# Performance work log

Measured on AMD Instinct MI355X. Metric: run time of the kernel, lower is better.

## Reference

```python
import math
import jax, jax.numpy as jnp
import numpy as np

FACTOR = 2  # init kwarg of AutoCorrelation


def setup_inputs() -> dict:
    key0 = jax.random.key(0)
    kq, kk, kv = jax.random.split(key0, 3)
    B, H, L, D = 8, 8, 2048, 64
    return {
        "query": jax.random.normal(kq, (B, H, L, D), dtype=jnp.float32),
        "key": jax.random.normal(kk, (B, H, L, D), dtype=jnp.float32),
        "value": jax.random.normal(kv, (B, H, L, D), dtype=jnp.float32),
    }


def reference(query, key, value):
    # Inference (eval-mode) path of AutoCorrelation.forward.
    B, H, L, D = query.shape
    L_KV = key.shape[2]
    # _pad_or_truncate_key_value: match key/value length to query length
    if L > L_KV:
        pad = [(0, 0), (0, 0), (0, L - L_KV), (0, 0)]
        key = jnp.pad(key, pad)
        value = jnp.pad(value, pad)
    else:
        key = key[:, :, :L, :]
        value = value[:, :, :L, :]

    # _period_based_dependency: circular cross-correlation via FFT
    qf = jnp.fft.rfft(jnp.swapaxes(query, -2, -1), axis=-1)   # (B,H,D,L//2+1) complex
    kf = jnp.fft.rfft(jnp.swapaxes(key, -2, -1), axis=-1)
    corr = jnp.fft.irfft(qf * jnp.conj(kf), n=L, axis=-1)     # (B,H,D,L)

    # _time_delay_aggregation (eval branch: per-batch topk delays)
    mean_corr = corr.mean(axis=(1, 2))                         # (B,L)
    num_delays = min(FACTOR * math.ceil(math.log(L)), L)
    w, delay_idx = jax.lax.top_k(mean_corr, num_delays)       # (B,k)
    w = jax.nn.softmax(w, axis=-1)

    ar = jnp.arange(L)

    def body(ctx, inp):
        d, wk = inp  # (B,), (B,)
        idx = (ar[None, :] + d[:, None]) % L                   # (B,L) — circular shift == gather from doubled value
        gathered = jnp.take_along_axis(
            value, jnp.broadcast_to(idx[:, None, :, None], value.shape), axis=2
        )                                                      # (B,H,L,D)
        return ctx + wk[:, None, None, None] * gathered, None

    ctx0 = jnp.zeros_like(value)
    context, _ = jax.lax.scan(body, ctx0, (delay_idx.T, w.T))
    return context
```

## Files before the change

### kernel.cpp

```cpp
#include <hip/hip_runtime.h>

static constexpr int LSEQ = 2048;
static constexpr int NB   = 8;
static constexpr int NH   = 8;
static constexpr int ND   = 64;
static constexpr int NDEL = 16;

static constexpr size_t WS_P_OFF     = 0;
static constexpr size_t WS_W_OFF     = 8388608;
static constexpr size_t WS_DELAY_OFF = 8389120;

__device__ __forceinline__ int SWZ(int x) { return x ^ (((x >> 4) & 7) << 1); }

__device__ __forceinline__ int pof(int f) {
    return ((f & 7) << 8) | (((f >> 3) & 7) << 5) | (((f >> 6) & 7) << 2) | (f >> 9);
}
__device__ __forceinline__ int fofp(int p) {
    return (p >> 8) | (((p >> 5) & 7) << 3) | (((p >> 2) & 7) << 6) | ((p & 3) << 9);
}

#define CMUL(ar, ai, br, bi) make_float2((ar)*(br) - (ai)*(bi), (ar)*(bi) + (ai)*(br))

__device__ __forceinline__ void dft8(const float2 x[8], float2 X[8]) {
    const float RH = 0.70710678118654752440f;
    float2 a0 = make_float2(x[0].x + x[4].x, x[0].y + x[4].y);
    float2 a1 = make_float2(x[1].x + x[5].x, x[1].y + x[5].y);
    float2 a2 = make_float2(x[2].x + x[6].x, x[2].y + x[6].y);
    float2 a3 = make_float2(x[3].x + x[7].x, x[3].y + x[7].y);
    float2 b0 = make_float2(x[0].x - x[4].x, x[0].y - x[4].y);
    float  t1r = x[1].x - x[5].x, t1i = x[1].y - x[5].y;
    float2 b1 = make_float2(RH * (t1r + t1i), RH * (t1i - t1r));
    float  t2r = x[2].x - x[6].x, t2i = x[2].y - x[6].y;
    float2 b2 = make_float2(t2i, -t2r);
    float  t3r = x[3].x - x[7].x, t3i = x[3].y - x[7].y;
    float2 b3 = make_float2(RH * (t3i - t3r), -RH * (t3r + t3i));
    float2 c0 = make_float2(a0.x + a2.x, a0.y + a2.y);
    float2 d0 = make_float2(a0.x - a2.x, a0.y - a2.y);
    float2 c1 = make_float2(a1.x + a3.x, a1.y + a3.y);
    float2 d1 = make_float2(a1.y - a3.y, -(a1.x - a3.x));
    X[0] = make_float2(c0.x + c1.x, c0.y + c1.y);
    X[4] = make_float2(c0.x - c1.x, c0.y - c1.y);
    X[2] = make_float2(d0.x + d1.x, d0.y + d1.y);
    X[6] = make_float2(d0.x - d1.x, d0.y - d1.y);
    float2 e0 = make_float2(b0.x + b2.x, b0.y + b2.y);
    float2 f0 = make_float2(b0.x - b2.x, b0.y - b2.y);
    float2 e1 = make_float2(b1.x + b3.x, b1.y + b3.y);
    float2 f1 = make_float2(b1.y - b3.y, -(b1.x - b3.x));
    X[1] = make_float2(e0.x + e1.x, e0.y + e1.y);
    X[5] = make_float2(e0.x - e1.x, e0.y - e1.y);
    X[3] = make_float2(f0.x + f1.x, f0.y + f1.y);
    X[7] = make_float2(f0.x - f1.x, f0.y - f1.y);
}

__device__ __forceinline__ void dft4(const float2 x[4], float2 X[4]) {
    float2 s0 = make_float2(x[0].x + x[2].x, x[0].y + x[2].y);
    float2 s1 = make_float2(x[1].x + x[3].x, x[1].y + x[3].y);
    float2 d0 = make_float2(x[0].x - x[2].x, x[0].y - x[2].y);
    float2 d1 = make_float2(x[1].y - x[3].y, -(x[1].x - x[3].x));
    X[0] = make_float2(s0.x + s1.x, s0.y + s1.y);
    X[2] = make_float2(s0.x - s1.x, s0.y - s1.y);
    X[1] = make_float2(d0.x + d1.x, d0.y + d1.y);
    X[3] = make_float2(d0.x - d1.x, d0.y - d1.y);
}

__global__ __launch_bounds__(256, 3) void fft_corr(const float* __restrict__ q,
                                                   const float* __restrict__ k,
                                                   float2* __restrict__ P) {
    __shared__ float2 z[LSEQ];
    const int t   = threadIdx.x;
    const int bi  = blockIdx.x;
    const int xcd = bi & 7;
    const int sl  = bi >> 3;
    const int bh  = xcd * 8 + (sl >> 3);
    const int grp = sl & 7;
    const int b   = bh >> 3;
    const int h   = bh & 7;
    const size_t base = (size_t)bh * LSEQ * ND + (size_t)(grp * 8);

    float2 WA[7], WB[7], WC[7];
    {
        float sn, cs;
        __sincosf(-6.28318530717958647692f * (float)t / 2048.f, &sn, &cs);
        WA[0] = make_float2(cs, sn);
        __sincosf(-6.28318530717958647692f * (float)(t & 31) / 256.f, &sn, &cs);
        WB[0] = make_float2(cs, sn);
        __sincosf(-6.28318530717958647692f * (float)(t & 3) / 32.f, &sn, &cs);
        WC[0] = make_float2(cs, sn);
        #pragma unroll
        for (int m = 1; m < 7; ++m) {
            WA[m] = CMUL(WA[m-1].x, WA[m-1].y, WA[0].x, WA[0].y);
            WB[m] = CMUL(WB[m-1].x, WB[m-1].y, WB[0].x, WB[0].y);
            WC[m] = CMUL(WC[m-1].x, WC[m-1].y, WC[0].x, WC[0].y);
        }
    }

    int fS[4], pmS[4];
    #pragma unroll
    for (int s = 0; s < 4; ++s) {
        const int cc = (s < 2) ? s : s + 2;
        const int f  = fofp(8 * t + cc);
        const int m  = (2048 - f) & 2047;
        fS[s]  = f;
        pmS[s] = SWZ(pof(m));
    }
    float aFr[4] = {0, 0, 0, 0}, aFi[4] = {0, 0, 0, 0};
    float aS = 0.f;

    const int sbB   = (t >> 5) * 256 + (t & 31);
    const int baseC = (t >> 2) * 32 + (t & 3);

    for (int half = 0; half < 2; ++half) {
        float4 qa[8], ka[8];
        #pragma unroll
        for (int j = 0; j < 8; ++j) {
            const size_t r = base + (size_t)(t + 256 * j) * ND + half * 4;
            qa[j] = *(const float4*)(q + r);
            ka[j] = *(const float4*)(k + r);
        }
        #pragma unroll
        for (int c = 0; c < 4; ++c) {
            float2 X[8], Y[8];
            #pragma unroll
            for (int j = 0; j < 8; ++j)
                X[j] = make_float2((&qa[j].x)[c], (&ka[j].x)[c]);

            __syncthreads();

            dft8(X, Y);
            #pragma unroll
            for (int m = 1; m < 8; ++m) Y[m] = CMUL(Y[m].x, Y[m].y, WA[m-1].x, WA[m-1].y);
            #pragma unroll
            for (int m = 0; m < 8; ++m) z[SWZ(m * 256 + t)] = Y[m];
            __syncthreads();

            {
                int adr[8];
                #pragma unroll
                for (int n = 0; n < 8; ++n) adr[n] = SWZ(sbB + 32 * n);
                #pragma unroll
                for (int j = 0; j < 8; ++j) X[j] = z[adr[j]];
                dft8(X, Y);
                #pragma unroll
                for (int m = 1; m < 8; ++m) Y[m] = CMUL(Y[m].x, Y[m].y, WB[m-1].x, WB[m-1].y);
                #pragma unroll
                for (int m = 0; m < 8; ++m) z[adr[m]] = Y[m];
            }
            __syncthreads();

            {
                int adr[8];
                #pragma unroll
                for (int n = 0; n < 8; ++n) adr[n] = SWZ(baseC + 4 * n);
                #pragma unroll
                for (int j = 0; j < 8; ++j) X[j] = z[adr[j]];
                dft8(X, Y);
                #pragma unroll
                for (int m = 1; m < 8; ++m) Y[m] = CMUL(Y[m].x, Y[m].y, WC[m-1].x, WC[m-1].y);
                #pragma unroll
                for (int m = 0; m < 8; ++m) z[adr[m]] = Y[m];
            }
            __syncthreads();

            {
                int adr[8];
                #pragma unroll
                for (int n = 0; n < 8; ++n) adr[n] = SWZ(8 * t + n);
                float2 xin[8];
                #pragma unroll
                for (int j = 0; j < 8; ++j) xin[j] = z[adr[j]];
                dft4(&xin[0], &X[0]);
                dft4(&xin[4], &X[4]);
                #pragma unroll
                for (int m = 0; m < 8; ++m) z[adr[m]] = X[m];
            }
            __syncthreads();

            #pragma unroll
            for (int s = 0; s < 4; ++s) {
                const int cc = (s < 2) ? s : s + 2;
                const float2 Zf = X[cc];
                const float2 Zm = z[pmS[s]];
                const float qr = 0.5f * (Zf.x + Zm.x), qi = 0.5f * (Zf.y - Zm.y);
                const float kr = 0.5f * (Zf.y + Zm.y), ki = 0.5f * (Zm.x - Zf.x);
                aFr[s] += qr * kr + qi * ki;
                aFi[s] += qi * kr - qr * ki;
            }
            if (t == 0) aS += X[2].x * X[2].y;
        }
    }

    const int part = h * 8 + grp;
    float2* Pp = P + (size_t)part * (NB * 2048) + (size_t)b * 2048;
    *(float4*)&Pp[8 * t]     = make_float4(aFr[0], aFi[0], aFr[1], aFi[1]);
    *(float4*)&Pp[8 * t + 4] = make_float4(aFr[2], aFi[2], aFr[3], aFi[3]);
    #pragma unroll
    for (int s = 0; s < 4; ++s) {
        const int m = (2048 - fS[s]) & 2047;
        if (m != fS[s]) Pp[pof(m)] = make_float2(aFr[s], -aFi[s]);
    }
    if (t == 0) Pp[pof(1024)] = make_float2(aS, 0.f);
}

__global__ __launch_bounds__(1024) void ifft_topk(const float2* __restrict__ P,
                                                  float* __restrict__ wout,
                                                  int* __restrict__ dout) {
    const int b = blockIdx.x, tid = threadIdx.x;
    __shared__ float2 y[LSEQ];
    __shared__ float  mc[LSEQ];
    __shared__ float  pv[16];
    __shared__ int    pi[16];
    __shared__ float  topv[NDEL];
    __shared__ int    topi[NDEL];

    float2 s0 = make_float2(0.f, 0.f), s1 = make_float2(0.f, 0.f);
    const float2* Pb = P + (size_t)b * 2048;
    #pragma unroll 8
    for (int part = 0; part < 64; ++part) {
        const float2 v0 = Pb[(size_t)part * (NB * 2048) + tid];
        const float2 v1 = Pb[(size_t)part * (NB * 2048) + tid + 1024];
        s0.x += v0.x; s0.y += v0.y; s1.x += v1.x; s1.y += v1.y;
    }
    y[__brev((unsigned)fofp(tid)) >> 21]        = s0;
    y[__brev((unsigned)fofp(tid + 1024)) >> 21] = s1;
    __syncthreads();

    for (int M = 2; M <= LSEQ; M <<= 1) {
        const int   half = M >> 1;
        const float w0   = 6.28318530717958647692f / (float)M;
        const int   kk = tid & (half - 1), i0 = 2 * tid - kk, i1 = i0 + half;
        const float2 a = y[i0], bb = y[i1];
        float sn, cs;
        __sincosf(w0 * (float)kk, &sn, &cs);
        const float tx = bb.x * cs - bb.y * sn, ty = bb.x * sn + bb.y * cs;
        y[i0] = make_float2(a.x + tx, a.y + ty);
        y[i1] = make_float2(a.x - tx, a.y - ty);
        __syncthreads();
    }

    const float scale = 1.0f / ((float)LSEQ * (float)(NH * ND));
    mc[tid]        = y[tid].x * scale;
    mc[tid + 1024] = y[tid + 1024].x * scale;
    __syncthreads();

    const int lane = tid & 63, wv = tid >> 6;
    for (int it = 0; it < NDEL; ++it) {
        const float v0 = mc[tid], v1 = mc[tid + 1024];
        float bv; int bix;
        if (v1 > v0) { bv = v1; bix = tid + 1024; } else { bv = v0; bix = tid; }
        #pragma unroll
        for (int off = 32; off; off >>= 1) {
            const float ov = __shfl_xor(bv, off);
            const int   oi = __shfl_xor(bix, off);
            if (ov > bv || (ov == bv && oi < bix)) { bv = ov; bix = oi; }
        }
        if (lane == 0) { pv[wv] = bv; pi[wv] = bix; }
        __syncthreads();
        if (tid < 64) {
            float v = (tid < 16) ? pv[tid] : -3e38f;
            int  ii = (tid < 16) ? pi[tid] : 0;
            #pragma unroll
            for (int off = 8; off; off >>= 1) {
                const float ov = __shfl_xor(v, off);
                const int   oi = __shfl_xor(ii, off);
                if (ov > v || (ov == v && oi < ii)) { v = ov; ii = oi; }
            }
            if (tid == 0) { topv[it] = v; topi[it] = ii; mc[ii] = -3e38f; }
        }
        __syncthreads();
    }

    if (tid == 0) {
        const float m = topv[0];
        float e[NDEL], sum = 0.f;
        for (int t2 = 0; t2 < NDEL; ++t2) { e[t2] = __expf(topv[t2] - m); sum += e[t2]; }
        const float inv = 1.0f / sum;
        for (int t2 = 0; t2 < NDEL; ++t2) {
            wout[b * NDEL + t2] = e[t2] * inv;
            dout[b * NDEL + t2] = topi[t2];
        }
    }
}

__global__ __launch_bounds__(256) void gather_out(const float* __restrict__ v,
                                                  const float* __restrict__ w,
                                                  const int* __restrict__ delay,
                                                  float* __restrict__ out) {
    const int bi  = blockIdx.x;
    const int xcd = bi & 7;
    const int s   = bi >> 3;
    const int bh  = xcd * 8 + (s >> 7);
    const int bt  = s & 127;
    const int b   = bh >> 3;
    const int tid = threadIdx.x;

    __shared__ float sw_[NDEL];
    __shared__ int   sd_[NDEL];
    if (tid < NDEL) {
        sw_[tid] = w[b * NDEL + tid];
        sd_[tid] = delay[b * NDEL + tid];
    }
    __syncthreads();

    const float* vb = v + (size_t)bh * LSEQ * ND;
    float*       ob = out + (size_t)bh * LSEQ * ND;

    const int row = tid >> 4;
    const int col = (tid & 15) * 4;
    const int t   = bt * 16 + row;

    float4 acc = make_float4(0.f, 0.f, 0.f, 0.f);
    #pragma unroll
    for (int kk = 0; kk < NDEL; ++kk) {
        const int r = (t + sd_[kk]) & (LSEQ - 1);
        const float4 vv = *(const float4*)(vb + (size_t)r * ND + col);
        const float wv = sw_[kk];
        acc.x += wv * vv.x; acc.y += wv * vv.y;
        acc.z += wv * vv.z; acc.w += wv * vv.w;
    }
    *(float4*)(ob + (size_t)t * ND + col) = acc;
}

extern "C" void kernel_launch(void* const* d_in, const int* in_sizes, int n_in,
                              void* d_out, int out_size, void* d_ws, size_t ws_size,
                              hipStream_t stream) {
    const float* q = (const float*)d_in[0];
    const float* k = (const float*)d_in[1];
    const float* v = (const float*)d_in[2];
    float* out = (float*)d_out;

    float2* P     = (float2*)((char*)d_ws + WS_P_OFF);
    float*  w     = (float*)((char*)d_ws + WS_W_OFF);
    int*    delay = (int*)((char*)d_ws + WS_DELAY_OFF);

    fft_corr<<<dim3(512), dim3(256), 0, stream>>>(q, k, P);
    ifft_topk<<<dim3(NB), dim3(1024), 0, stream>>>(P, w, delay);
    gather_out<<<dim3(NB * NH * 128), dim3(256), 0, stream>>>(v, w, delay, out);
}
```

Baseline: 226.7 us.

## Batch two FFT columns per sync in fft_corr and split reduction from inverse FFT

fft_corr now processes two columns at a time in two shared buffers, which halves the number of barriers per column and adds ILP. Occupancy is lowered to 2 blocks per CU because of the doubled LDS and register use. The 64-part reduction moves into a separate 64-block kernel so it is no longer done by only 8 blocks. The inverse FFT becomes a 256-thread radix-8 Stockham pass that reuses the forward stages, replacing the 11-stage radix-2 loop with a sync per stage. This adds one extra kernel launch.

```diff
diff --git a/kernel.cpp b/kernel.cpp
--- a/kernel.cpp
+++ b/kernel.cpp
@@ -63,10 +63,31 @@
     X[3] = make_float2(d0.x - d1.x, d0.y - d1.y);
 }
 
-__global__ __launch_bounds__(256, 3) void fft_corr(const float* __restrict__ q,
+__device__ __forceinline__ void stageR8(float2* zp, const int adr[8], const float2 W[7]) {
+    float2 X[8], Y[8];
+    #pragma unroll
+    for (int j = 0; j < 8; ++j) X[j] = zp[adr[j]];
+    dft8(X, Y);
+    #pragma unroll
+    for (int m = 1; m < 8; ++m) Y[m] = CMUL(Y[m].x, Y[m].y, W[m-1].x, W[m-1].y);
+    #pragma unroll
+    for (int m = 0; m < 8; ++m) zp[adr[m]] = Y[m];
+}
+
+__device__ __forceinline__ void stageD(float2* zp, const int adr[8], float2 X[8]) {
+    float2 xin[8];
+    #pragma unroll
+    for (int j = 0; j < 8; ++j) xin[j] = zp[adr[j]];
+    dft4(&xin[0], &X[0]);
+    dft4(&xin[4], &X[4]);
+    #pragma unroll
+    for (int m = 0; m < 8; ++m) zp[adr[m]] = X[m];
+}
+
+__global__ __launch_bounds__(256, 2) void fft_corr(const float* __restrict__ q,
                                                    const float* __restrict__ k,
                                                    float2* __restrict__ P) {
-    __shared__ float2 z[LSEQ];
+    __shared__ float2 z0[LSEQ], z1[LSEQ];
     const int t   = threadIdx.x;
     const int bi  = blockIdx.x;
     const int xcd = bi & 7;
@@ -108,7 +129,15 @@
 
     const int sbB   = (t >> 5) * 256 + (t & 31);
     const int baseC = (t >> 2) * 32 + (t & 3);
-
+    int adrB[8], adrC[8], adrD[8];
+    #pragma unroll
+    for (int n = 0; n < 8; ++n) {
+        adrB[n] = SWZ(sbB + 32 * n);
+        adrC[n] = SWZ(baseC + 4 * n);
+        adrD[n] = SWZ(8 * t + n);
+    }
+
+    #pragma unroll
     for (int half = 0; half < 2; ++half) {
         float4 qa[8], ka[8];
         #pragma unroll
@@ -118,74 +147,62 @@
             ka[j] = *(const float4*)(k + r);
         }
         #pragma unroll
-        for (int c = 0; c < 4; ++c) {
-            float2 X[8], Y[8];
+        for (int pr = 0; pr < 2; ++pr) {
+            const int c0 = 2 * pr, c1 = 2 * pr + 1;
+            float2 X0[8], X1[8], Y0[8], Y1[8];
             #pragma unroll
-            for (int j = 0; j < 8; ++j)
-                X[j] = make_float2((&qa[j].x)[c], (&ka[j].x)[c]);
-
-            __syncthreads();
-
-            dft8(X, Y);
-            #pragma unroll
-            for (int m = 1; m < 8; ++m) Y[m] = CMUL(Y[m].x, Y[m].y, WA[m-1].x, WA[m-1].y);
-            #pragma unroll
-            for (int m = 0; m < 8; ++m) z[SWZ(m * 256 + t)] = Y[m];
-            __syncthreads();
-
-            {
-                int adr[8];
-                #pragma unroll
-                for (int n = 0; n < 8; ++n) adr[n] = SWZ(sbB + 32 * n);
-                #pragma unroll
-                for (int j = 0; j < 8; ++j) X[j] = z[adr[j]];
-                dft8(X, Y);
-                #pragma unroll
-                for (int m = 1; m < 8; ++m) Y[m] = CMUL(Y[m].x, Y[m].y, WB[m-1].x, WB[m-1].y);
-                #pragma unroll
-                for (int m = 0; m < 8; ++m) z[adr[m]] = Y[m];
+            for (int j = 0; j < 8; ++j) {
+                X0[j] = make_float2((&qa[j].x)[c0], (&ka[j].x)[c0]);
+                X1[j] = make_float2((&qa[j].x)[c1], (&ka[j].x)[c1]);
             }
             __syncthreads();
 
-            {
-                int adr[8];
-                #pragma unroll
-                for (int n = 0; n < 8; ++n) adr[n] = SWZ(baseC + 4 * n);
-                #pragma unroll
-                for (int j = 0; j < 8; ++j) X[j] = z[adr[j]];
-                dft8(X, Y);
-                #pragma unroll
-                for (int m = 1; m < 8; ++m) Y[m] = CMUL(Y[m].x, Y[m].y, WC[m-1].x, WC[m-1].y);
-                #pragma unroll
-                for (int m = 0; m < 8; ++m) z[adr[m]] = Y[m];
+            dft8(X0, Y0);
+            dft8(X1, Y1);
+            #pragma unroll
+            for (int m = 1; m < 8; ++m) {
+                Y0[m] = CMUL(Y0[m].x, Y0[m].y, WA[m-1].x, WA[m-1].y);
+                Y1[m] = CMUL(Y1[m].x, Y1[m].y, WA[m-1].x, WA[m-1].y);
+            }
+            #pragma unroll
+            for (int m = 0; m < 8; ++m) {
+                const int a = SWZ(m * 256 + t);
+                z0[a] = Y0[m];
+                z1[a] = Y1[m];
             }
             __syncthreads();
 
-            {
-                int adr[8];
-                #pragma unroll
-                for (int n = 0; n < 8; ++n) adr[n] = SWZ(8 * t + n);
-                float2 xin[8];
-                #pragma unroll
-                for (int j = 0; j < 8; ++j) xin[j] = z[adr[j]];
-                dft4(&xin[0], &X[0]);
-                dft4(&xin[4], &X[4]);
-                #pragma unroll
-                for (int m = 0; m < 8; ++m) z[adr[m]] = X[m];
-            }
+            stageR8(z0, adrB, WB);
+            stageR8(z1, adrB, WB);
+            __syncthreads();
+
+            stageR8(z0, adrC, WC);
+            stageR8(z1, adrC, WC);
+            __syncthreads();
+
+            stageD(z0, adrD, X0);
+            stageD(z1, adrD, X1);
             __syncthreads();
 
             #pragma unroll
             for (int s = 0; s < 4; ++s) {
                 const int cc = (s < 2) ? s : s + 2;
-                const float2 Zf = X[cc];
-                const float2 Zm = z[pmS[s]];
-                const float qr = 0.5f * (Zf.x + Zm.x), qi = 0.5f * (Zf.y - Zm.y);
-                const float kr = 0.5f * (Zf.y + Zm.y), ki = 0.5f * (Zm.x - Zf.x);
-                aFr[s] += qr * kr + qi * ki;
-                aFi[s] += qi * kr - qr * ki;
+                {
+                    const float2 Zf = X0[cc], Zm = z0[pmS[s]];
+                    const float qr = 0.5f * (Zf.x + Zm.x), qi = 0.5f * (Zf.y - Zm.y);
+                    const float kr = 0.5f * (Zf.y + Zm.y), ki = 0.5f * (Zm.x - Zf.x);
+                    aFr[s] += qr * kr + qi * ki;
+                    aFi[s] += qi * kr - qr * ki;
+                }
+                {
+                    const float2 Zf = X1[cc], Zm = z1[pmS[s]];
+                    const float qr = 0.5f * (Zf.x + Zm.x), qi = 0.5f * (Zf.y - Zm.y);
+                    const float kr = 0.5f * (Zf.y + Zm.y), ki = 0.5f * (Zm.x - Zf.x);
+                    aFr[s] += qr * kr + qi * ki;
+                    aFi[s] += qi * kr - qr * ki;
+                }
             }
-            if (t == 0) aS += X[2].x * X[2].y;
+            if (t == 0) aS += X0[2].x * X0[2].y + X1[2].x * X1[2].y;
         }
     }
 
@@ -201,82 +218,130 @@
     if (t == 0) Pp[pof(1024)] = make_float2(aS, 0.f);
 }
 
-__global__ __launch_bounds__(1024) void ifft_topk(const float2* __restrict__ P,
-                                                  float* __restrict__ wout,
-                                                  int* __restrict__ dout) {
-    const int b = blockIdx.x, tid = threadIdx.x;
-    __shared__ float2 y[LSEQ];
+__global__ __launch_bounds__(256) void reduce_S(float2* __restrict__ P) {
+    const int g = blockIdx.x * 256 + threadIdx.x;
+    float ax = 0.f, ay = 0.f;
+    #pragma unroll 8
+    for (int part = 0; part < 64; ++part) {
+        const float2 v = P[(size_t)part * (NB * 2048) + g];
+        ax += v.x; ay += v.y;
+    }
+    P[g] = make_float2(ax, ay);
+}
+
+__global__ __launch_bounds__(256) void ifft_topk(const float2* __restrict__ S,
+                                                 float* __restrict__ wout,
+                                                 int* __restrict__ dout) {
+    __shared__ float2 zz[LSEQ];
     __shared__ float  mc[LSEQ];
-    __shared__ float  pv[16];
-    __shared__ int    pi[16];
+    __shared__ float  pv[4];
+    __shared__ int    pig[4];
     __shared__ float  topv[NDEL];
     __shared__ int    topi[NDEL];
-
-    float2 s0 = make_float2(0.f, 0.f), s1 = make_float2(0.f, 0.f);
-    const float2* Pb = P + (size_t)b * 2048;
-    #pragma unroll 8
-    for (int part = 0; part < 64; ++part) {
-        const float2 v0 = Pb[(size_t)part * (NB * 2048) + tid];
-        const float2 v1 = Pb[(size_t)part * (NB * 2048) + tid + 1024];
-        s0.x += v0.x; s0.y += v0.y; s1.x += v1.x; s1.y += v1.y;
-    }
-    y[__brev((unsigned)fofp(tid)) >> 21]        = s0;
-    y[__brev((unsigned)fofp(tid + 1024)) >> 21] = s1;
-    __syncthreads();
-
-    for (int M = 2; M <= LSEQ; M <<= 1) {
-        const int   half = M >> 1;
-        const float w0   = 6.28318530717958647692f / (float)M;
-        const int   kk = tid & (half - 1), i0 = 2 * tid - kk, i1 = i0 + half;
-        const float2 a = y[i0], bb = y[i1];
+    const int b = blockIdx.x, t = threadIdx.x;
+
+    float2 WA[7], WB[7], WC[7];
+    {
         float sn, cs;
-        __sincosf(w0 * (float)kk, &sn, &cs);
-        const float tx = bb.x * cs - bb.y * sn, ty = bb.x * sn + bb.y * cs;
-        y[i0] = make_float2(a.x + tx, a.y + ty);
-        y[i1] = make_float2(a.x - tx, a.y - ty);
-        __syncthreads();
+        __sincosf(-6.28318530717958647692f * (float)t / 2048.f, &sn, &cs);
+        WA[0] = make_float2(cs, sn);
+        __sincosf(-6.28318530717958647692f * (float)(t & 31) / 256.f, &sn, &cs);
+        WB[0] = make_float2(cs, sn);
+        __sincosf(-6.28318530717958647692f * (float)(t & 3) / 32.f, &sn, &cs);
+        WC[0] = make_float2(cs, sn);
+        #pragma unroll
+        for (int m = 1; m < 7; ++m) {
+            WA[m] = CMUL(WA[m-1].x, WA[m-1].y, WA[0].x, WA[0].y);
+            WB[m] = CMUL(WB[m-1].x, WB[m-1].y, WB[0].x, WB[0].y);
+            WC[m] = CMUL(WC[m-1].x, WC[m-1].y, WC[0].x, WC[0].y);
+        }
+    }
+    const int sbB   = (t >> 5) * 256 + (t & 31);
+    const int baseC = (t >> 2) * 32 + (t & 3);
+    int adrB[8], adrC[8], adrD[8];
+    #pragma unroll
+    for (int n = 0; n < 8; ++n) {
+        adrB[n] = SWZ(sbB + 32 * n);
+        adrC[n] = SWZ(baseC + 4 * n);
+        adrD[n] = SWZ(8 * t + n);
+    }
+
+    #pragma unroll
+    for (int j = 0; j < 8; ++j) zz[t + 256 * j] = S[b * 2048 + t + 256 * j];
+    __syncthreads();
+
+    float2 X[8], Y[8];
+    #pragma unroll
+    for (int j = 0; j < 8; ++j) {
+        const float2 s = zz[pof(t + 256 * j)];
+        X[j] = make_float2(s.x, -s.y);
+    }
+    __syncthreads();
+
+    dft8(X, Y);
+    #pragma unroll
+    for (int m = 1; m < 8; ++m) Y[m] = CMUL(Y[m].x, Y[m].y, WA[m-1].x, WA[m-1].y);
+    #pragma unroll
+    for (int m = 0; m < 8; ++m) zz[SWZ(m * 256 + t)] = Y[m];
+    __syncthreads();
+
+    stageR8(zz, adrB, WB);
+    __syncthreads();
+    stageR8(zz, adrC, WC);
+    __syncthreads();
+
+    {
+        float2 xin[8];
+        #pragma unroll
+        for (int j = 0; j < 8; ++j) xin[j] = zz[adrD[j]];
+        dft4(&xin[0], &X[0]);
+        dft4(&xin[4], &X[4]);
     }
 
     const float scale = 1.0f / ((float)LSEQ * (float)(NH * ND));
-    mc[tid]        = y[tid].x * scale;
-    mc[tid + 1024] = y[tid + 1024].x * scale;
-    __syncthreads();
-
-    const int lane = tid & 63, wv = tid >> 6;
+    #pragma unroll
+    for (int cc = 0; cc < 8; ++cc) mc[fofp(8 * t + cc)] = X[cc].x * scale;
+    __syncthreads();
+
+    const int lane = t & 63, wv = t >> 6;
     for (int it = 0; it < NDEL; ++it) {
-        const float v0 = mc[tid], v1 = mc[tid + 1024];
-        float bv; int bix;
-        if (v1 > v0) { bv = v1; bix = tid + 1024; } else { bv = v0; bix = tid; }
+        float bv = -3e38f; int bix = 0;
+        #pragma unroll
+        for (int u = 0; u < 8; ++u) {
+            const int idx = t + 256 * u;
+            const float v = mc[idx];
+            if (v > bv || (v == bv && idx < bix)) { bv = v; bix = idx; }
+        }
         #pragma unroll
         for (int off = 32; off; off >>= 1) {
             const float ov = __shfl_xor(bv, off);
             const int   oi = __shfl_xor(bix, off);
             if (ov > bv || (ov == bv && oi < bix)) { bv = ov; bix = oi; }
         }
-        if (lane == 0) { pv[wv] = bv; pi[wv] = bix; }
+        if (lane == 0) { pv[wv] = bv; pig[wv] = bix; }
         __syncthreads();
-        if (tid < 64) {
-            float v = (tid < 16) ? pv[tid] : -3e38f;
-            int  ii = (tid < 16) ? pi[tid] : 0;
+        if (t < 64) {
+            float v = (t < 4) ? pv[t] : -3e38f;
+            int  ii = (t < 4) ? pig[t] : 0;
             #pragma unroll
-            for (int off = 8; off; off >>= 1) {
+            for (int off = 2; off; off >>= 1) {
                 const float ov = __shfl_xor(v, off);
                 const int   oi = __shfl_xor(ii, off);
                 if (ov > v || (ov == v && oi < ii)) { v = ov; ii = oi; }
             }
-            if (tid == 0) { topv[it] = v; topi[it] = ii; mc[ii] = -3e38f; }
+            if (t == 0) { topv[it] = v; topi[it] = ii; mc[ii] = -3e38f; }
         }
         __syncthreads();
     }
 
-    if (tid == 0) {
+    if (t == 0) {
         const float m = topv[0];
         float e[NDEL], sum = 0.f;
-        for (int t2 = 0; t2 < NDEL; ++t2) { e[t2] = __expf(topv[t2] - m); sum += e[t2]; }
+        for (int i = 0; i < NDEL; ++i) { e[i] = __expf(topv[i] - m); sum += e[i]; }
         const float inv = 1.0f / sum;
-        for (int t2 = 0; t2 < NDEL; ++t2) {
-            wout[b * NDEL + t2] = e[t2] * inv;
-            dout[b * NDEL + t2] = topi[t2];
+        for (int i = 0; i < NDEL; ++i) {
+            wout[b * NDEL + i] = e[i] * inv;
+            dout[b * NDEL + i] = topi[i];
         }
     }
 }
@@ -333,6 +398,7 @@
     int*    delay = (int*)((char*)d_ws + WS_DELAY_OFF);
 
     fft_corr<<<dim3(512), dim3(256), 0, stream>>>(q, k, P);
-    ifft_topk<<<dim3(NB), dim3(1024), 0, stream>>>(P, w, delay);
+    reduce_S<<<dim3(64), dim3(256), 0, stream>>>(P);
+    ifft_topk<<<dim3(NB), dim3(256), 0, stream>>>(P, w, delay);
     gather_out<<<dim3(NB * NH * 128), dim3(256), 0, stream>>>(v, w, delay, out);
 }
```

Measured after the change: 200.2 us. 1.13x faster.
